# Performance work log

Hardware: AMD Instinct MI355X
Metric: run time of the kernel (lower is better)

## Reference

```python
import jax, jax.numpy as jnp
import numpy as np

B, L, D = 16, 1024, 1024
H = 8
K = D // H
OUT = 64

def setup_inputs() -> dict:
    key = jax.random.key(0)
    ks = jax.random.split(key, 12)
    std = 0.1
    return {
        "x0": jax.random.normal(ks[0], (B, L, D), jnp.float32),
        "x1": jax.random.normal(ks[1], (B, L, D), jnp.float32),
        "x2": jax.random.normal(ks[2], (B, L, D), jnp.float32),
        "support": jax.random.normal(ks[3], (B, L), jnp.float32),
        "mask": jnp.ones((B, L), jnp.float32),
        "Wk": std * jax.random.normal(ks[4], (D, D), jnp.float32),   # tokeys.weight
        "Wq": std * jax.random.normal(ks[5], (D, D), jnp.float32),   # toqueries.weight
        "Wv": std * jax.random.normal(ks[6], (D, D), jnp.float32),   # tovalues.weight
        "Wu": std * jax.random.normal(ks[7], (D, D), jnp.float32),   # unifyheads.weight
        "bu": std * jax.random.normal(ks[8], (D,), jnp.float32),     # unifyheads.bias
        "Wmlp": std * jax.random.normal(ks[9], (OUT, D), jnp.float32),
        "bmlp": std * jax.random.normal(ks[10], (OUT,), jnp.float32),
    }

def reference(x0, x1, x2, support, mask, Wk, Wq, Wv, Wu, bu, Wmlp, bmlp):
    # SelfAttention with first=True: q from x2 via tokeys, k from x1 via toqueries, v from x0 via tovalues
    b, l, d = x0.shape
    h, k = H, K
    scale = k ** (-0.25)  # applied to both q and k, as in the torch code
    q = (x2 @ Wk.T).reshape(b, l, h, k) * scale
    key_ = (x1 @ Wq.T).reshape(b, l, h, k) * scale
    v = (x0 @ Wv.T).reshape(b, l, h, k)
    dot = jnp.einsum('blhk,bmhk->bhlm', q, key_)          # [b,h,l,l]
    attn = jax.nn.softmax(dot, axis=-1)
    out = jnp.einsum('bhlm,bmhk->blhk', attn, v).reshape(b, l, d)
    out = out @ Wu.T + bu                                  # unifyheads
    pooled = jnp.mean(out, axis=1) + jnp.max(out, axis=1)  # 'mean_and_max'
    logits = pooled @ Wmlp.T + bmlp                        # dropout = identity (eval)
    return logits
```

## Files before the change

### kernel.cpp

```cpp
#include <hip/hip_runtime.h>

using u16 = unsigned short;
using u32 = unsigned int;
using short8 = __attribute__((ext_vector_type(8))) short;
using floatx4 = __attribute__((ext_vector_type(4))) float;

__device__ __forceinline__ u32 fbits(float f) { union { float f; u32 u; } v; v.f = f; return v.u; }
__device__ __forceinline__ float fofb(u32 u) { union { u32 u; float f; } v; v.u = u; return v.f; }

__device__ __forceinline__ u16 f2bf(float f) {
    u32 u = fbits(f);
    return (u16)((u + 0x7FFFu + ((u >> 16) & 1u)) >> 16);
}

__device__ __forceinline__ void cvt_split8(const float* x, short8& h, short8& l) {
#pragma unroll
    for (int j = 0; j < 8; ++j) {
        u32 b = fbits(x[j]);
        h[j] = (short)(b >> 16);
        float r = x[j] - fofb(b & 0xffff0000u);
        l[j] = (short)(fbits(r) >> 16);
    }
}
__device__ __forceinline__ void cvt_rne8(const float* x, short8& h) {
#pragma unroll
    for (int j = 0; j < 8; ++j) h[j] = (short)f2bf(x[j]);
}

__device__ __forceinline__ void load_lds16(const void* g, u16* l) {
    __builtin_amdgcn_global_load_lds(
        (const __attribute__((address_space(1))) unsigned int*)(g),
        (__attribute__((address_space(3))) unsigned int*)(l), 16, 0, 0);
}

__global__ void convw_kernel(const float* __restrict__ W0, const float* __restrict__ W1,
                             const float* __restrict__ W2, const float* __restrict__ W3,
                             u16* __restrict__ D0, u16* __restrict__ D1,
                             u16* __restrict__ D2, u16* __restrict__ D3) {
    int y = blockIdx.y;
    const float* s = (y == 0) ? W0 : (y == 1) ? W1 : (y == 2) ? W2 : W3;
    u16* d = (y == 0) ? D0 : (y == 1) ? D1 : (y == 2) ? D2 : D3;
    int i = (blockIdx.x * 256 + threadIdx.x) * 4;
    float4 v = *reinterpret_cast<const float4*>(s + i);
    ushort4 h;
    h.x = f2bf(v.x); h.y = f2bf(v.y); h.z = f2bf(v.z); h.w = f2bf(v.w);
    *reinterpret_cast<ushort4*>(d + i) = h;
}

#define GK 1024
#define GN 1024

template<bool SPLIT, bool TRANS, bool POOL, bool FP32A>
__global__ __launch_bounds__(256)
void gemm_bt(const void* __restrict__ Av, const u16* __restrict__ Bh,
             u16* __restrict__ Cb, float scale, u16* __restrict__ Vt,
             float* __restrict__ psum, float* __restrict__ pmax)
{
    constexpr int SM = TRANS ? 17408 : (FP32A ? 12288 : 8192);
    __shared__ __align__(16) u16 smem[SM];

    const int tid  = threadIdx.x;
    const int lane = tid & 63, wave = tid >> 6;
    const int quad = lane >> 4, l15 = lane & 15;
    const int wr = wave >> 1, wc = wave & 1;
    const int bm = blockIdx.y * 128, bn = blockIdx.x * 128;

    const int BOff = FP32A ? 8192 : 4096;

    floatx4 acc[4][4];
#pragma unroll
    for (int mt = 0; mt < 4; ++mt)
#pragma unroll
        for (int nt = 0; nt < 4; ++nt)
#pragma unroll
            for (int r = 0; r < 4; ++r) acc[mt][nt][r] = 0.f;

    const int s8 = (quad ^ ((l15 >> 1) & 3)) * 8;

    for (int kt = 0; kt < GK; kt += 32) {
        __syncthreads();
        if (FP32A) {
            const float* Af = (const float*)Av;
            const int arow = lane >> 3, achk = (lane & 7) ^ (lane >> 3);
            const int brow = lane >> 2, bchk = (lane & 3) ^ ((lane >> 3) & 3);
#pragma unroll
            for (int j = 0; j < 6; ++j) {
                int n = wave + 4 * j;
                if (n < 16) {
                    load_lds16(Af + (size_t)(bm + n * 8 + arow) * GK + kt + achk * 4,
                               smem + n * 512);
                } else {
                    int m = n - 16;
                    load_lds16(Bh + (size_t)(bn + m * 16 + brow) * GK + kt + bchk * 8,
                               smem + 8192 + m * 512);
                }
            }
        } else {
            const u16* Ab = (const u16*)Av;
            const int cgl = (lane & 3) ^ ((lane >> 3) & 3);
            const int rl  = lane >> 2;
            const u16* gp = (wave < 2) ? Ab : Bh;
            int rowb = (wave < 2) ? bm : bn;
            u16* lp = smem + (wave >> 1) * 4096;
            int q0 = (wave & 1) * 4;
#pragma unroll
            for (int q = 0; q < 4; ++q) {
                int qq = q0 + q;
                load_lds16(gp + (size_t)(rowb + qq * 16 + rl) * GK + cgl * 8 + kt,
                           lp + qq * 512);
            }
        }
        __syncthreads();

        short8 a_h[4], a_l[4], b_h[4];
        if (FP32A) {
            const float* Af4 = (const float*)smem;
#pragma unroll
            for (int mt = 0; mt < 4; ++mt) {
                int ra = wr * 64 + mt * 16 + l15;
                int f = ra & 7;
                float xv[8];
                *reinterpret_cast<float4*>(xv) =
                    *reinterpret_cast<const float4*>(Af4 + ra * 32 + (((2 * quad) ^ f) * 4));
                *reinterpret_cast<float4*>(xv + 4) =
                    *reinterpret_cast<const float4*>(Af4 + ra * 32 + (((2 * quad + 1) ^ f) * 4));
                if (SPLIT) cvt_split8(xv, a_h[mt], a_l[mt]);
                else       cvt_rne8(xv, a_h[mt]);
            }
        } else {
#pragma unroll
            for (int mt = 0; mt < 4; ++mt) {
                int ra = wr * 64 + mt * 16 + l15;
                a_h[mt] = *reinterpret_cast<const short8*>(smem + ra * 32 + s8);
            }
        }
#pragma unroll
        for (int nt = 0; nt < 4; ++nt) {
            int rb = wc * 64 + nt * 16 + l15;
            b_h[nt] = *reinterpret_cast<const short8*>(smem + BOff + rb * 32 + s8);
        }
#pragma unroll
        for (int mt = 0; mt < 4; ++mt)
#pragma unroll
            for (int nt = 0; nt < 4; ++nt)
                acc[mt][nt] = __builtin_amdgcn_mfma_f32_16x16x32_bf16(a_h[mt], b_h[nt], acc[mt][nt], 0, 0, 0);
        if (SPLIT) {
#pragma unroll
            for (int mt = 0; mt < 4; ++mt)
#pragma unroll
                for (int nt = 0; nt < 4; ++nt)
                    acc[mt][nt] = __builtin_amdgcn_mfma_f32_16x16x32_bf16(a_l[mt], b_h[nt], acc[mt][nt], 0, 0, 0);
        }
    }

    if (POOL) {
#pragma unroll
        for (int nt = 0; nt < 4; ++nt) {
            float s = 0.f, m = -3.0e38f;
#pragma unroll
            for (int mt = 0; mt < 4; ++mt)
#pragma unroll
                for (int r = 0; r < 4; ++r) {
                    float v = acc[mt][nt][r];
                    s += v; m = fmaxf(m, v);
                }
            s += __shfl_xor(s, 16); s += __shfl_xor(s, 32);
            m = fmaxf(m, __shfl_xor(m, 16)); m = fmaxf(m, __shfl_xor(m, 32));
            if (quad == 0) {
                int col = bn + wc * 64 + nt * 16 + l15;
                int chunk = blockIdx.y * 2 + wr;
                psum[chunk * 1024 + col] = s;
                pmax[chunk * 1024 + col] = m;
            }
        }
    } else if (!TRANS) {
#pragma unroll
        for (int mt = 0; mt < 4; ++mt)
#pragma unroll
            for (int nt = 0; nt < 4; ++nt)
#pragma unroll
                for (int r = 0; r < 4; ++r) {
                    int row = bm + wr * 64 + mt * 16 + quad * 4 + r;
                    int col = bn + wc * 64 + nt * 16 + l15;
                    Cb[(size_t)row * GN + col] = f2bf(acc[mt][nt][r] * scale);
                }
    } else {
        __syncthreads();
#pragma unroll
        for (int mt = 0; mt < 4; ++mt)
#pragma unroll
            for (int nt = 0; nt < 4; ++nt)
#pragma unroll
                for (int r = 0; r < 4; ++r) {
                    int row_local = wr * 64 + mt * 16 + quad * 4 + r;
                    int col_local = wc * 64 + nt * 16 + l15;
                    smem[col_local * 136 + row_local] = f2bf(acc[mt][nt][r]);
                }
        __syncthreads();
        int b = bm >> 10, l0 = bm & 1023, h = blockIdx.x;
        int d = tid >> 1, rblk = (tid & 1) * 64;
        u16* gv = Vt + ((size_t)(b * 8 + h) * 128 + d) * 1024 + l0 + rblk;
#pragma unroll
        for (int v = 0; v < 8; ++v)
            *reinterpret_cast<short8*>(gv + v * 8) =
                *reinterpret_cast<const short8*>(smem + d * 136 + rblk + v * 8);
    }
}

#define LOG2E 1.44269504088896f
#define EXPC  46.1662413084470f

__global__ __launch_bounds__(256)
void attn_kernel(const u16* __restrict__ Q, const u16* __restrict__ Kk,
                 const u16* __restrict__ Vt, u16* __restrict__ AO)
{
    __shared__ __align__(16) u16 Ks[64 * 128];
    __shared__ __align__(16) u16 Vts[128 * 64];
    __shared__ __align__(16) u16 Ps[4][16 * 64];

    const int tid  = threadIdx.x;
    const int lane = tid & 63, wave = tid >> 6;
    const int quad = lane >> 4, l15 = lane & 15;
    const int l7 = l15 & 7;
    const int qt = blockIdx.x, h = blockIdx.y, b = blockIdx.z;

    short8 qf[4];
    {
        int qrow = b * 1024 + qt * 64 + wave * 16 + l15;
        const u16* qp = Q + (size_t)qrow * 1024 + h * 128;
#pragma unroll
        for (int s = 0; s < 4; ++s)
            qf[s] = *reinterpret_cast<const short8*>(qp + s * 32 + quad * 8);
    }

    float lsum = 0.f;
    floatx4 oacc[8];
#pragma unroll
    for (int nt = 0; nt < 8; ++nt)
#pragma unroll
        for (int r = 0; r < 4; ++r) oacc[nt][r] = 0.f;

    const int krow_l = lane >> 4;
    const u16* kgB[4];
#pragma unroll
    for (int i = 0; i < 4; ++i) {
        int cg = (lane & 15) ^ ((i * 4 + krow_l) & 7);
        kgB[i] = Kk + (size_t)(b * 1024 + wave * 16 + i * 4 + krow_l) * 1024
                    + h * 128 + cg * 8;
    }
    const u16* vtb = Vt + (size_t)(b * 8 + h) * 128 * 1024;
    const int vrow_l = lane >> 3;
    const u16* vgB = vtb + (size_t)(wave * 32 + vrow_l) * 1024
                         + (((lane & 7) ^ vrow_l) * 8);

    for (int kt2 = 0; kt2 < 16; ++kt2) {
        __syncthreads();
#pragma unroll
        for (int i = 0; i < 4; ++i)
            load_lds16(kgB[i] + (size_t)kt2 * 64 * 1024, Ks + (wave * 16 + i * 4) * 128);
#pragma unroll
        for (int i = 0; i < 4; ++i)
            load_lds16(vgB + (size_t)i * 8 * 1024 + kt2 * 64, Vts + (wave * 32 + i * 8) * 64);
        __syncthreads();

        floatx4 sacc[4];
#pragma unroll
        for (int nt = 0; nt < 4; ++nt)
#pragma unroll
            for (int r = 0; r < 4; ++r) sacc[nt][r] = 0.f;
#pragma unroll
        for (int s = 0; s < 4; ++s)
#pragma unroll
            for (int nt = 0; nt < 4; ++nt) {
                short8 kfr = *reinterpret_cast<const short8*>(
                    &Ks[(nt * 16 + l15) * 128 + ((s * 4 + quad) ^ l7) * 8]);
                sacc[nt] = __builtin_amdgcn_mfma_f32_16x16x32_bf16(kfr, qf[s], sacc[nt], 0, 0, 0);
            }

#pragma unroll
        for (int nt = 0; nt < 4; ++nt) {
            float p0 = exp2f(fmaf(sacc[nt][0], LOG2E, -EXPC));
            float p1 = exp2f(fmaf(sacc[nt][1], LOG2E, -EXPC));
            float p2 = exp2f(fmaf(sacc[nt][2], LOG2E, -EXPC));
            float p3 = exp2f(fmaf(sacc[nt][3], LOG2E, -EXPC));
            lsum += (p0 + p1) + (p2 + p3);
            uint2 w;
            w.x = (unsigned)f2bf(p0) | ((unsigned)f2bf(p1) << 16);
            w.y = (unsigned)f2bf(p2) | ((unsigned)f2bf(p3) << 16);
            int ch = nt * 2 + (quad >> 1);
            *reinterpret_cast<uint2*>(
                &Ps[wave][l15 * 64 + (ch ^ l7) * 8 + (quad & 1) * 4]) = w;
        }

#pragma unroll
        for (int ks = 0; ks < 2; ++ks) {
            short8 pa = *reinterpret_cast<const short8*>(
                &Ps[wave][l15 * 64 + ((ks * 4 + quad) ^ l7) * 8]);
#pragma unroll
            for (int nt = 0; nt < 8; ++nt) {
                short8 bv = *reinterpret_cast<const short8*>(
                    &Vts[(nt * 16 + l15) * 64 + ((ks * 4 + quad) ^ l7) * 8]);
                oacc[nt] = __builtin_amdgcn_mfma_f32_16x16x32_bf16(pa, bv, oacc[nt], 0, 0, 0);
            }
        }
    }

    lsum += __shfl_xor(lsum, 16);
    lsum += __shfl_xor(lsum, 32);

#pragma unroll
    for (int r = 0; r < 4; ++r) {
        float inv = 1.0f / __shfl(lsum, quad * 4 + r);
        int row = b * 1024 + qt * 64 + wave * 16 + quad * 4 + r;
#pragma unroll
        for (int nt = 0; nt < 8; ++nt) {
            int col = h * 128 + nt * 16 + l15;
            AO[(size_t)row * 1024 + col] = f2bf(oacc[nt][r] * inv);
        }
    }
}

__global__ __launch_bounds__(256)
void head_kernel(const float* __restrict__ psum, const float* __restrict__ pmax,
                 const float* __restrict__ bu, const float* __restrict__ Wmlp,
                 const float* __restrict__ bmlp, float* __restrict__ out) {
    __shared__ float pool_s[1024];
    int b = blockIdx.x, tid = threadIdx.x;
    int c4 = tid * 4;
    float4 s = {0.f, 0.f, 0.f, 0.f};
    float4 m = {-3.0e38f, -3.0e38f, -3.0e38f, -3.0e38f};
#pragma unroll
    for (int c = 0; c < 16; ++c) {
        float4 a = *reinterpret_cast<const float4*>(psum + (size_t)(b * 16 + c) * 1024 + c4);
        float4 x = *reinterpret_cast<const float4*>(pmax + (size_t)(b * 16 + c) * 1024 + c4);
        s.x += a.x; s.y += a.y; s.z += a.z; s.w += a.w;
        m.x = fmaxf(m.x, x.x); m.y = fmaxf(m.y, x.y);
        m.z = fmaxf(m.z, x.z); m.w = fmaxf(m.w, x.w);
    }
    float4 bb = *reinterpret_cast<const float4*>(bu + c4);
    pool_s[c4 + 0] = s.x * (1.0f / 1024.0f) + m.x + 2.0f * bb.x;
    pool_s[c4 + 1] = s.y * (1.0f / 1024.0f) + m.y + 2.0f * bb.y;
    pool_s[c4 + 2] = s.z * (1.0f / 1024.0f) + m.z + 2.0f * bb.z;
    pool_s[c4 + 3] = s.w * (1.0f / 1024.0f) + m.w + 2.0f * bb.w;
    __syncthreads();
    int o = tid >> 2, seg = tid & 3;
    const float4* wr = reinterpret_cast<const float4*>(Wmlp + o * 1024 + seg * 256);
    const float4* pr = reinterpret_cast<const float4*>(pool_s + seg * 256);
    float acc = 0.f;
#pragma unroll 8
    for (int i = 0; i < 64; ++i) {
        float4 a = pr[i], w = wr[i];
        acc += a.x * w.x + a.y * w.y + a.z * w.z + a.w * w.w;
    }
    acc += __shfl_xor(acc, 1);
    acc += __shfl_xor(acc, 2);
    if (seg == 0) out[b * 64 + o] = acc + bmlp[o];
}

extern "C" void kernel_launch(void* const* d_in, const int* in_sizes, int n_in,
                              void* d_out, int out_size, void* d_ws, size_t ws_size,
                              hipStream_t stream) {
    const float* x0 = (const float*)d_in[0];
    const float* x1 = (const float*)d_in[1];
    const float* x2 = (const float*)d_in[2];
    const float* Wk = (const float*)d_in[5];
    const float* Wq = (const float*)d_in[6];
    const float* Wv = (const float*)d_in[7];
    const float* Wu = (const float*)d_in[8];
    const float* bu = (const float*)d_in[9];
    const float* Wmlp = (const float*)d_in[10];
    const float* bmlp = (const float*)d_in[11];
    float* out = (float*)d_out;

    char* ws = (char*)d_ws;
    const size_t MB32 = 33554432ull;
    size_t wo = 0;
    u16* Wkh = (u16*)(ws + wo); wo += 2097152;
    u16* Wqh = (u16*)(ws + wo); wo += 2097152;
    u16* Wvh = (u16*)(ws + wo); wo += 2097152;
    u16* Wuh = (u16*)(ws + wo); wo += 2097152;
    u16* Qb = (u16*)(ws + wo); wo += MB32;
    u16* Kb = (u16*)(ws + wo); wo += MB32;
    u16* Vt = (u16*)(ws + wo); wo += MB32;
    u16* AOb = (u16*)(ws + wo); wo += MB32;
    float* psum = (float*)(ws + wo); wo += 1048576;
    float* pmax = (float*)(ws + wo); wo += 1048576;
    if (ws_size < wo) return;

    const float scale = 0.29730177875068026f;

    convw_kernel<<<dim3(1024, 4), 256, 0, stream>>>(Wk, Wq, Wv, Wu, Wkh, Wqh, Wvh, Wuh);

    dim3 ggrid(8, 128);
    gemm_bt<true, false, false, true><<<ggrid, 256, 0, stream>>>(x2, Wkh, Qb, scale, nullptr, nullptr, nullptr);
    gemm_bt<true, false, false, true><<<ggrid, 256, 0, stream>>>(x1, Wqh, Kb, scale, nullptr, nullptr, nullptr);
    gemm_bt<false, true, false, true><<<ggrid, 256, 0, stream>>>(x0, Wvh, nullptr, 1.0f, Vt, nullptr, nullptr);

    dim3 agrid(16, 8, 16);
    attn_kernel<<<agrid, 256, 0, stream>>>(Qb, Kb, Vt, AOb);

    gemm_bt<false, false, true, false><<<ggrid, 256, 0, stream>>>(AOb, Wuh, nullptr, 1.0f, nullptr, psum, pmax);

    head_kernel<<<16, 256, 0, stream>>>(psum, pmax, bu, Wmlp, bmlp, out);
}
```

Baseline: 650.5 us.

## Repartition attention waves over key columns and swap GEMM grid order

Result: no change. 643.6 us (-1.1%).

```diff
diff --git a/kernel.cpp b/kernel.cpp
--- a/kernel.cpp
+++ b/kernel.cpp
@@ -63,7 +63,7 @@
     const int lane = tid & 63, wave = tid >> 6;
     const int quad = lane >> 4, l15 = lane & 15;
     const int wr = wave >> 1, wc = wave & 1;
-    const int bm = blockIdx.y * 128, bn = blockIdx.x * 128;
+    const int bm = blockIdx.x * 128, bn = blockIdx.y * 128;
 
     const int BOff = FP32A ? 8192 : 4096;
 
@@ -168,7 +168,7 @@
             m = fmaxf(m, __shfl_xor(m, 16)); m = fmaxf(m, __shfl_xor(m, 32));
             if (quad == 0) {
                 int col = bn + wc * 64 + nt * 16 + l15;
-                int chunk = blockIdx.y * 2 + wr;
+                int chunk = (bm >> 6) + wr;
                 psum[chunk * 1024 + col] = s;
                 pmax[chunk * 1024 + col] = m;
             }
@@ -197,7 +197,7 @@
                     smem[col_local * 136 + row_local] = f2bf(acc[mt][nt][r]);
                 }
         __syncthreads();
-        int b = bm >> 10, l0 = bm & 1023, h = blockIdx.x;
+        int b = bm >> 10, l0 = bm & 1023, h = bn >> 7;
         int d = tid >> 1, rblk = (tid & 1) * 64;
         u16* gv = Vt + ((size_t)(b * 8 + h) * 128 + d) * 1024 + l0 + rblk;
 #pragma unroll
@@ -216,7 +216,7 @@
 {
     __shared__ __align__(16) u16 Ks[64 * 128];
     __shared__ __align__(16) u16 Vts[128 * 64];
-    __shared__ __align__(16) u16 Ps[4][16 * 64];
+    __shared__ __align__(16) u16 Ps[64 * 64];
 
     const int tid  = threadIdx.x;
     const int lane = tid & 63, wave = tid >> 6;
@@ -224,21 +224,24 @@
     const int l7 = l15 & 7;
     const int qt = blockIdx.x, h = blockIdx.y, b = blockIdx.z;
 
-    short8 qf[4];
-    {
-        int qrow = b * 1024 + qt * 64 + wave * 16 + l15;
+    short8 qf[4][4];
+#pragma unroll
+    for (int mt = 0; mt < 4; ++mt) {
+        int qrow = b * 1024 + qt * 64 + mt * 16 + l15;
         const u16* qp = Q + (size_t)qrow * 1024 + h * 128;
 #pragma unroll
         for (int s = 0; s < 4; ++s)
-            qf[s] = *reinterpret_cast<const short8*>(qp + s * 32 + quad * 8);
-    }
-
-    float lsum = 0.f;
-    floatx4 oacc[8];
-#pragma unroll
-    for (int nt = 0; nt < 8; ++nt)
-#pragma unroll
-        for (int r = 0; r < 4; ++r) oacc[nt][r] = 0.f;
+            qf[mt][s] = *reinterpret_cast<const short8*>(qp + s * 32 + quad * 8);
+    }
+
+    float lsum[4] = {0.f, 0.f, 0.f, 0.f};
+    floatx4 oacc[4][2];
+#pragma unroll
+    for (int mt = 0; mt < 4; ++mt)
+#pragma unroll
+        for (int ntl = 0; ntl < 2; ++ntl)
+#pragma unroll
+            for (int r = 0; r < 4; ++r) oacc[mt][ntl][r] = 0.f;
 
     const int krow_l = lane >> 4;
     const u16* kgB[4];
@@ -265,59 +268,80 @@
 
         floatx4 sacc[4];
 #pragma unroll
-        for (int nt = 0; nt < 4; ++nt)
-#pragma unroll
-            for (int r = 0; r < 4; ++r) sacc[nt][r] = 0.f;
-#pragma unroll
-        for (int s = 0; s < 4; ++s)
-#pragma unroll
-            for (int nt = 0; nt < 4; ++nt) {
-                short8 kfr = *reinterpret_cast<const short8*>(
-                    &Ks[(nt * 16 + l15) * 128 + ((s * 4 + quad) ^ l7) * 8]);
-                sacc[nt] = __builtin_amdgcn_mfma_f32_16x16x32_bf16(kfr, qf[s], sacc[nt], 0, 0, 0);
-            }
-
-#pragma unroll
-        for (int nt = 0; nt < 4; ++nt) {
-            float p0 = exp2f(fmaf(sacc[nt][0], LOG2E, -EXPC));
-            float p1 = exp2f(fmaf(sacc[nt][1], LOG2E, -EXPC));
-            float p2 = exp2f(fmaf(sacc[nt][2], LOG2E, -EXPC));
-            float p3 = exp2f(fmaf(sacc[nt][3], LOG2E, -EXPC));
-            lsum += (p0 + p1) + (p2 + p3);
+        for (int mt = 0; mt < 4; ++mt)
+#pragma unroll
+            for (int r = 0; r < 4; ++r) sacc[mt][r] = 0.f;
+#pragma unroll
+        for (int s = 0; s < 4; ++s) {
+            short8 kfr = *reinterpret_cast<const short8*>(
+                &Ks[(wave * 16 + l15) * 128 + ((s * 4 + quad) ^ l7) * 8]);
+#pragma unroll
+            for (int mt = 0; mt < 4; ++mt)
+                sacc[mt] = __builtin_amdgcn_mfma_f32_16x16x32_bf16(kfr, qf[mt][s], sacc[mt], 0, 0, 0);
+        }
+
+#pragma unroll
+        for (int mt = 0; mt < 4; ++mt) {
+            float p0 = exp2f(fmaf(sacc[mt][0], LOG2E, -EXPC));
+            float p1 = exp2f(fmaf(sacc[mt][1], LOG2E, -EXPC));
+            float p2 = exp2f(fmaf(sacc[mt][2], LOG2E, -EXPC));
+            float p3 = exp2f(fmaf(sacc[mt][3], LOG2E, -EXPC));
+            lsum[mt] += (p0 + p1) + (p2 + p3);
             uint2 w;
             w.x = (unsigned)f2bf(p0) | ((unsigned)f2bf(p1) << 16);
             w.y = (unsigned)f2bf(p2) | ((unsigned)f2bf(p3) << 16);
-            int ch = nt * 2 + (quad >> 1);
+            int ch = wave * 2 + (quad >> 1);
             *reinterpret_cast<uint2*>(
-                &Ps[wave][l15 * 64 + (ch ^ l7) * 8 + (quad & 1) * 4]) = w;
-        }
+                &Ps[(mt * 16 + l15) * 64 + (ch ^ l7) * 8 + (quad & 1) * 4]) = w;
+        }
+        __syncthreads();
 
 #pragma unroll
         for (int ks = 0; ks < 2; ++ks) {
-            short8 pa = *reinterpret_cast<const short8*>(
-                &Ps[wave][l15 * 64 + ((ks * 4 + quad) ^ l7) * 8]);
-#pragma unroll
-            for (int nt = 0; nt < 8; ++nt) {
+            short8 pa[4];
+#pragma unroll
+            for (int mt = 0; mt < 4; ++mt)
+                pa[mt] = *reinterpret_cast<const short8*>(
+                    &Ps[(mt * 16 + l15) * 64 + ((ks * 4 + quad) ^ l7) * 8]);
+#pragma unroll
+            for (int ntl = 0; ntl < 2; ++ntl) {
                 short8 bv = *reinterpret_cast<const short8*>(
-                    &Vts[(nt * 16 + l15) * 64 + ((ks * 4 + quad) ^ l7) * 8]);
-                oacc[nt] = __builtin_amdgcn_mfma_f32_16x16x32_bf16(pa, bv, oacc[nt], 0, 0, 0);
-            }
-        }
-    }
-
-    lsum += __shfl_xor(lsum, 16);
-    lsum += __shfl_xor(lsum, 32);
-
-#pragma unroll
-    for (int r = 0; r < 4; ++r) {
-        float inv = 1.0f / __shfl(lsum, quad * 4 + r);
-        int row = b * 1024 + qt * 64 + wave * 16 + quad * 4 + r;
-#pragma unroll
-        for (int nt = 0; nt < 8; ++nt) {
-            int col = h * 128 + nt * 16 + l15;
-            AO[(size_t)row * 1024 + col] = f2bf(oacc[nt][r] * inv);
-        }
-    }
+                    &Vts[((wave * 2 + ntl) * 16 + l15) * 64 + ((ks * 4 + quad) ^ l7) * 8]);
+#pragma unroll
+                for (int mt = 0; mt < 4; ++mt)
+                    oacc[mt][ntl] = __builtin_amdgcn_mfma_f32_16x16x32_bf16(pa[mt], bv, oacc[mt][ntl], 0, 0, 0);
+            }
+        }
+    }
+
+#pragma unroll
+    for (int mt = 0; mt < 4; ++mt) {
+        lsum[mt] += __shfl_xor(lsum[mt], 16);
+        lsum[mt] += __shfl_xor(lsum[mt], 32);
+    }
+    __syncthreads();
+    float* lred = (float*)Ps;
+    if (quad == 0) {
+#pragma unroll
+        for (int mt = 0; mt < 4; ++mt)
+            lred[(mt * 16 + l15) * 4 + wave] = lsum[mt];
+    }
+    __syncthreads();
+
+#pragma unroll
+    for (int mt = 0; mt < 4; ++mt)
+#pragma unroll
+        for (int r = 0; r < 4; ++r) {
+            int q = mt * 16 + quad * 4 + r;
+            float4 v = *reinterpret_cast<const float4*>(&lred[q * 4]);
+            float inv = 1.0f / ((v.x + v.y) + (v.z + v.w));
+            int row = b * 1024 + qt * 64 + q;
+#pragma unroll
+            for (int ntl = 0; ntl < 2; ++ntl) {
+                int col = h * 128 + wave * 32 + ntl * 16 + l15;
+                AO[(size_t)row * 1024 + col] = f2bf(oacc[mt][ntl][r] * inv);
+            }
+        }
 }
 
 __global__ __launch_bounds__(256)
@@ -391,7 +415,7 @@
 
     convw_kernel<<<dim3(1024, 4), 256, 0, stream>>>(Wk, Wq, Wv, Wu, Wkh, Wqh, Wvh, Wuh);
 
-    dim3 ggrid(8, 128);
+    dim3 ggrid(128, 8);
     gemm_bt<true, false, false, true><<<ggrid, 256, 0, stream>>>(x2, Wkh, Qb, scale, nullptr, nullptr, nullptr);
     gemm_bt<true, false, false, true><<<ggrid, 256, 0, stream>>>(x1, Wqh, Kb, scale, nullptr, nullptr, nullptr);
     gemm_bt<false, true, false, true><<<ggrid, 256, 0, stream>>>(x0, Wvh, nullptr, 1.0f, Vt, nullptr, nullptr);
```

## Switch attention to 32x32 MFMA with 128-query tiles and reorder GEMM grid

Applied to the files above, without the earlier changes.

After: 619.8 us. 4.7% less time.

```diff
diff --git a/kernel.cpp b/kernel.cpp
--- a/kernel.cpp
+++ b/kernel.cpp
@@ -4,6 +4,7 @@
 using u32 = unsigned int;
 using short8 = __attribute__((ext_vector_type(8))) short;
 using floatx4 = __attribute__((ext_vector_type(4))) float;
+using floatx16 = __attribute__((ext_vector_type(16))) float;
 
 __device__ __forceinline__ u32 fbits(float f) { union { float f; u32 u; } v; v.f = f; return v.u; }
 __device__ __forceinline__ float fofb(u32 u) { union { u32 u; float f; } v; v.u = u; return v.f; }
@@ -63,7 +64,7 @@
     const int lane = tid & 63, wave = tid >> 6;
     const int quad = lane >> 4, l15 = lane & 15;
     const int wr = wave >> 1, wc = wave & 1;
-    const int bm = blockIdx.y * 128, bn = blockIdx.x * 128;
+    const int bm = blockIdx.x * 128, bn = blockIdx.y * 128;
 
     const int BOff = FP32A ? 8192 : 4096;
 
@@ -168,7 +169,7 @@
             m = fmaxf(m, __shfl_xor(m, 16)); m = fmaxf(m, __shfl_xor(m, 32));
             if (quad == 0) {
                 int col = bn + wc * 64 + nt * 16 + l15;
-                int chunk = blockIdx.y * 2 + wr;
+                int chunk = (bm >> 6) + wr;
                 psum[chunk * 1024 + col] = s;
                 pmax[chunk * 1024 + col] = m;
             }
@@ -197,7 +198,7 @@
                     smem[col_local * 136 + row_local] = f2bf(acc[mt][nt][r]);
                 }
         __syncthreads();
-        int b = bm >> 10, l0 = bm & 1023, h = blockIdx.x;
+        int b = bm >> 10, l0 = bm & 1023, h = bn >> 7;
         int d = tid >> 1, rblk = (tid & 1) * 64;
         u16* gv = Vt + ((size_t)(b * 8 + h) * 128 + d) * 1024 + l0 + rblk;
 #pragma unroll
@@ -216,29 +217,29 @@
 {
     __shared__ __align__(16) u16 Ks[64 * 128];
     __shared__ __align__(16) u16 Vts[128 * 64];
-    __shared__ __align__(16) u16 Ps[4][16 * 64];
+    __shared__ __align__(16) u16 Ps[4][32 * 64];
 
     const int tid  = threadIdx.x;
     const int lane = tid & 63, wave = tid >> 6;
-    const int quad = lane >> 4, l15 = lane & 15;
-    const int l7 = l15 & 7;
-    const int qt = blockIdx.x, h = blockIdx.y, b = blockIdx.z;
-
-    short8 qf[4];
+    const int l31 = lane & 31, h2 = lane >> 5;
+    const int l7 = lane & 7;
+    const int qt = blockIdx.x, hd = blockIdx.y, b = blockIdx.z;
+
+    short8 qf[8];
     {
-        int qrow = b * 1024 + qt * 64 + wave * 16 + l15;
-        const u16* qp = Q + (size_t)qrow * 1024 + h * 128;
-#pragma unroll
-        for (int s = 0; s < 4; ++s)
-            qf[s] = *reinterpret_cast<const short8*>(qp + s * 32 + quad * 8);
+        int qrow = b * 1024 + qt * 128 + wave * 32 + l31;
+        const u16* qp = Q + (size_t)qrow * 1024 + hd * 128 + h2 * 8;
+#pragma unroll
+        for (int s = 0; s < 8; ++s)
+            qf[s] = *reinterpret_cast<const short8*>(qp + s * 16);
     }
 
     float lsum = 0.f;
-    floatx4 oacc[8];
-#pragma unroll
-    for (int nt = 0; nt < 8; ++nt)
-#pragma unroll
-        for (int r = 0; r < 4; ++r) oacc[nt][r] = 0.f;
+    floatx16 oacc[4];
+#pragma unroll
+    for (int db = 0; db < 4; ++db)
+#pragma unroll
+        for (int r = 0; r < 16; ++r) oacc[db][r] = 0.f;
 
     const int krow_l = lane >> 4;
     const u16* kgB[4];
@@ -246,9 +247,9 @@
     for (int i = 0; i < 4; ++i) {
         int cg = (lane & 15) ^ ((i * 4 + krow_l) & 7);
         kgB[i] = Kk + (size_t)(b * 1024 + wave * 16 + i * 4 + krow_l) * 1024
-                    + h * 128 + cg * 8;
-    }
-    const u16* vtb = Vt + (size_t)(b * 8 + h) * 128 * 1024;
+                    + hd * 128 + cg * 8;
+    }
+    const u16* vtb = Vt + (size_t)(b * 8 + hd) * 128 * 1024;
     const int vrow_l = lane >> 3;
     const u16* vgB = vtb + (size_t)(wave * 32 + vrow_l) * 1024
                          + (((lane & 7) ^ vrow_l) * 8);
@@ -263,61 +264,61 @@
             load_lds16(vgB + (size_t)i * 8 * 1024 + kt2 * 64, Vts + (wave * 32 + i * 8) * 64);
         __syncthreads();
 
-        floatx4 sacc[4];
-#pragma unroll
-        for (int nt = 0; nt < 4; ++nt)
-#pragma unroll
-            for (int r = 0; r < 4; ++r) sacc[nt][r] = 0.f;
-#pragma unroll
-        for (int s = 0; s < 4; ++s)
-#pragma unroll
-            for (int nt = 0; nt < 4; ++nt) {
+#pragma unroll
+        for (int kb = 0; kb < 2; ++kb) {
+            floatx16 sacc;
+#pragma unroll
+            for (int r = 0; r < 16; ++r) sacc[r] = 0.f;
+#pragma unroll
+            for (int s = 0; s < 8; ++s) {
+                int key = kb * 32 + l31;
                 short8 kfr = *reinterpret_cast<const short8*>(
-                    &Ks[(nt * 16 + l15) * 128 + ((s * 4 + quad) ^ l7) * 8]);
-                sacc[nt] = __builtin_amdgcn_mfma_f32_16x16x32_bf16(kfr, qf[s], sacc[nt], 0, 0, 0);
-            }
-
-#pragma unroll
-        for (int nt = 0; nt < 4; ++nt) {
-            float p0 = exp2f(fmaf(sacc[nt][0], LOG2E, -EXPC));
-            float p1 = exp2f(fmaf(sacc[nt][1], LOG2E, -EXPC));
-            float p2 = exp2f(fmaf(sacc[nt][2], LOG2E, -EXPC));
-            float p3 = exp2f(fmaf(sacc[nt][3], LOG2E, -EXPC));
-            lsum += (p0 + p1) + (p2 + p3);
-            uint2 w;
-            w.x = (unsigned)f2bf(p0) | ((unsigned)f2bf(p1) << 16);
-            w.y = (unsigned)f2bf(p2) | ((unsigned)f2bf(p3) << 16);
-            int ch = nt * 2 + (quad >> 1);
-            *reinterpret_cast<uint2*>(
-                &Ps[wave][l15 * 64 + (ch ^ l7) * 8 + (quad & 1) * 4]) = w;
-        }
-
-#pragma unroll
-        for (int ks = 0; ks < 2; ++ks) {
-            short8 pa = *reinterpret_cast<const short8*>(
-                &Ps[wave][l15 * 64 + ((ks * 4 + quad) ^ l7) * 8]);
-#pragma unroll
-            for (int nt = 0; nt < 8; ++nt) {
-                short8 bv = *reinterpret_cast<const short8*>(
-                    &Vts[(nt * 16 + l15) * 64 + ((ks * 4 + quad) ^ l7) * 8]);
-                oacc[nt] = __builtin_amdgcn_mfma_f32_16x16x32_bf16(pa, bv, oacc[nt], 0, 0, 0);
-            }
-        }
-    }
-
-    lsum += __shfl_xor(lsum, 16);
+                    &Ks[key * 128 + (((s * 2 + h2) ^ l7) * 8)]);
+                sacc = __builtin_amdgcn_mfma_f32_32x32x16_bf16(kfr, qf[s], sacc, 0, 0, 0);
+            }
+#pragma unroll
+            for (int rg = 0; rg < 4; ++rg) {
+                float p0 = exp2f(fmaf(sacc[rg * 4 + 0], LOG2E, -EXPC));
+                float p1 = exp2f(fmaf(sacc[rg * 4 + 1], LOG2E, -EXPC));
+                float p2 = exp2f(fmaf(sacc[rg * 4 + 2], LOG2E, -EXPC));
+                float p3 = exp2f(fmaf(sacc[rg * 4 + 3], LOG2E, -EXPC));
+                lsum += (p0 + p1) + (p2 + p3);
+                uint2 w;
+                w.x = (unsigned)f2bf(p0) | ((unsigned)f2bf(p1) << 16);
+                w.y = (unsigned)f2bf(p2) | ((unsigned)f2bf(p3) << 16);
+                *reinterpret_cast<uint2*>(
+                    &Ps[wave][l31 * 64 + ((kb * 4 + rg) ^ l7) * 8 + 4 * h2]) = w;
+            }
+        }
+
+#pragma unroll
+        for (int ks = 0; ks < 4; ++ks) {
+            short8 pfr = *reinterpret_cast<const short8*>(
+                &Ps[wave][l31 * 64 + (((ks * 2 + h2) ^ l7) * 8)]);
+#pragma unroll
+            for (int db = 0; db < 4; ++db) {
+                int d = db * 32 + l31;
+                short8 vfr = *reinterpret_cast<const short8*>(
+                    &Vts[d * 64 + (((ks * 2 + h2) ^ l7) * 8)]);
+                oacc[db] = __builtin_amdgcn_mfma_f32_32x32x16_bf16(pfr, vfr, oacc[db], 0, 0, 0);
+            }
+        }
+    }
+
     lsum += __shfl_xor(lsum, 32);
 
-#pragma unroll
-    for (int r = 0; r < 4; ++r) {
-        float inv = 1.0f / __shfl(lsum, quad * 4 + r);
-        int row = b * 1024 + qt * 64 + wave * 16 + quad * 4 + r;
-#pragma unroll
-        for (int nt = 0; nt < 8; ++nt) {
-            int col = h * 128 + nt * 16 + l15;
-            AO[(size_t)row * 1024 + col] = f2bf(oacc[nt][r] * inv);
-        }
-    }
+    int qbase = b * 1024 + qt * 128 + wave * 32;
+#pragma unroll
+    for (int rg = 0; rg < 4; ++rg)
+#pragma unroll
+        for (int r = 0; r < 4; ++r) {
+            int row = rg * 8 + 4 * h2 + r;
+            float inv = 1.0f / __shfl(lsum, row);
+            u16* ao = AO + (size_t)(qbase + row) * 1024 + hd * 128 + l31;
+#pragma unroll
+            for (int db = 0; db < 4; ++db)
+                ao[db * 32] = f2bf(oacc[db][rg * 4 + r] * inv);
+        }
 }
 
 __global__ __launch_bounds__(256)
@@ -391,12 +392,12 @@
 
     convw_kernel<<<dim3(1024, 4), 256, 0, stream>>>(Wk, Wq, Wv, Wu, Wkh, Wqh, Wvh, Wuh);
 
-    dim3 ggrid(8, 128);
+    dim3 ggrid(128, 8);
     gemm_bt<true, false, false, true><<<ggrid, 256, 0, stream>>>(x2, Wkh, Qb, scale, nullptr, nullptr, nullptr);
     gemm_bt<true, false, false, true><<<ggrid, 256, 0, stream>>>(x1, Wqh, Kb, scale, nullptr, nullptr, nullptr);
     gemm_bt<false, true, false, true><<<ggrid, 256, 0, stream>>>(x0, Wvh, nullptr, 1.0f, Vt, nullptr, nullptr);
 
-    dim3 agrid(16, 8, 16);
+    dim3 agrid(8, 8, 16);
     attn_kernel<<<agrid, 256, 0, stream>>>(Qb, Kb, Vt, AOb);
 
     gemm_bt<false, false, true, false><<<ggrid, 256, 0, stream>>>(AOb, Wuh, nullptr, 1.0f, nullptr, psum, pmax);
```
